# Kernel tuning notes

Measured on AMD Instinct MI355X. Metric: run time of the kernel, lower is better.

## Reference

```python
import jax, jax.numpy as jnp
import numpy as np

HIDDEN, NH, NKV, HD = 2048, 16, 2, 128
CTX, NL, POS = 4096, 36, 3000
THETA, EPS = 1.0e6, 1e-6


def _rope_cos_sin(pos):
    inv_freq = 1.0 / (THETA ** (jnp.arange(0, HD, 2, dtype=jnp.float32) / HD))  # [HD/2]
    ang = pos * inv_freq
    ang = jnp.concatenate([ang, ang])  # [HD]
    return jnp.cos(ang), jnp.sin(ang)


def _rotate_half(x):
    x1, x2 = x[..., : HD // 2], x[..., HD // 2 :]
    return jnp.concatenate([-x2, x1], axis=-1)


def setup_inputs() -> dict:
    key = jax.random.key(0)
    ks = jax.random.split(key, 12)
    w = lambda k, shape, s=0.02: (jax.random.normal(k, shape, dtype=jnp.float32) * s)
    mask = jnp.where(jnp.arange(CTX) <= POS, 0.0, -1e9).astype(jnp.float32).reshape(1, 1, 1, CTX)
    return {
        "hidden_states": jax.random.normal(ks[0], (1, 1, HIDDEN), dtype=jnp.float32),
        "position_ids": jnp.array([POS], dtype=jnp.int64 if jax.config.jax_enable_x64 else jnp.int32),
        "causal_mask": mask,
        "current_pos": POS,
        "ln_w": jnp.ones((HIDDEN,), jnp.float32) + w(ks[1], (HIDDEN,)),
        "wq": w(ks[2], (NH * HD, HIDDEN)),
        "bq": w(ks[3], (NH * HD,)),
        "wk": w(ks[4], (NKV * HD, HIDDEN)),
        "bk": w(ks[5], (NKV * HD,)),
        "wv": w(ks[6], (NKV * HD, HIDDEN)),
        "bv": w(ks[7], (NKV * HD,)),
        "wo": w(ks[8], (HIDDEN, NH * HD)),
        "kv_cache": w(ks[9], (2 * NL, NKV, CTX, HD), 1.0),
    }


def reference(hidden_states, position_ids, causal_mask, current_pos,
              ln_w, wq, bq, wk, bk, wv, bv, wo, kv_cache):
    x = hidden_states  # [1,1,H]
    # RMSNorm
    var = jnp.mean(x * x, axis=-1, keepdims=True)
    nx = x * jax.lax.rsqrt(var + EPS) * ln_w

    # QKV projections (single token)
    t = nx[0, 0]  # [H]
    q = (wq @ t + bq).reshape(NH, HD)    # [NH, HD]
    k = (wk @ t + bk).reshape(NKV, HD)   # [NKV, HD]
    v = (wv @ t + bv).reshape(NKV, HD)

    # RoPE at current position
    cos, sin = _rope_cos_sin(jnp.float32(current_pos))
    q = q * cos + _rotate_half(q) * sin
    k = k * cos + _rotate_half(k) * sin

    # KV-cache scatter write: key at layer slot 0, value at slot NL
    kv_cache = kv_cache.at[0, :, current_pos, :].set(k)
    kv_cache = kv_cache.at[NL, :, current_pos, :].set(v)
    key_cache = kv_cache[0]    # [NKV, CTX, HD]
    value_cache = kv_cache[NL]

    # GQA attention over full cache
    rep = NH // NKV
    K = jnp.repeat(key_cache, rep, axis=0)    # [NH, CTX, HD]
    V = jnp.repeat(value_cache, rep, axis=0)
    scores = jnp.einsum("hd,hkd->hk", q, K) / jnp.sqrt(jnp.float32(HD))
    scores = scores + causal_mask[0, 0, 0]    # [NH, CTX]
    probs = jax.nn.softmax(scores, axis=-1)
    ctx = jnp.einsum("hk,hkd->hd", probs, V)  # [NH, HD]
    attn_out = (wo @ ctx.reshape(NH * HD)).reshape(1, 1, HIDDEN)

    return hidden_states + attn_out
```

## Files before the change

kernel.cpp:

```cpp
#include <hip/hip_runtime.h>
#include <hip/hip_bf16.h>
#include <math.h>

#define HIDDEN 2048
#define NH 16
#define NKV 2
#define HD 128
#define CTX 4096
#define NL 36
#define EPS 1e-6f

#define CHUNK 128
#define NCHUNKS (CTX / CHUNK)
#define HPB 4
#define NGRP (NH / HPB)

#define WS_QRAW 0
#define WS_KRAW 2048
#define WS_VRAW 2304
#define WS_TAB  2560
#define WS_PML  2688
#define WS_PACC 3712

#define RSQRT_HD 0.08838834764831845f

__device__ __forceinline__ float dot4(float4 a, float4 b) {
    return a.x*b.x + a.y*b.y + a.z*b.z + a.w*b.w;
}

__global__ __launch_bounds__(256) void qkv_kernel(
    const float* __restrict__ x, const float* __restrict__ lnw,
    const float* __restrict__ wq, const float* __restrict__ bq,
    const float* __restrict__ wk, const float* __restrict__ bk,
    const float* __restrict__ wv, const float* __restrict__ bv,
    const int* __restrict__ curpos, float* __restrict__ ws)
{
    const int t = threadIdx.x;
    const int lane = t & 63, wid = t >> 6;

    if (blockIdx.x == 320) {
        if (t < 64) {
            double e = (double)t * (1.0 / 64.0);
            double invf = exp2(-19.931568569324174087 * e);
            double a = (double)curpos[0] * invf;
            a -= 6.2831853071795864769 * floor(a * 0.15915494309189533577);
            float s, c;
            sincosf((float)a, &s, &c);
            ws[WS_TAB + t] = c;
            ws[WS_TAB + 64 + t] = s;
        }
        return;
    }

    const int R0 = blockIdx.x * 8 + wid * 2;
    const float *w0, *w1; float b0, b1; float *dst0, *dst1;
    {
        int R = R0;
        if (R < 2048)      { w0 = wq + (size_t)R * HIDDEN;            b0 = bq[R];   dst0 = ws + WS_QRAW + R; }
        else if (R < 2304) { int r = R - 2048; w0 = wk + (size_t)r * HIDDEN; b0 = bk[r]; dst0 = ws + WS_KRAW + r; }
        else               { int r = R - 2304; w0 = wv + (size_t)r * HIDDEN; b0 = bv[r]; dst0 = ws + WS_VRAW + r; }
        R = R0 + 1;
        if (R < 2048)      { w1 = wq + (size_t)R * HIDDEN;            b1 = bq[R];   dst1 = ws + WS_QRAW + R; }
        else if (R < 2304) { int r = R - 2048; w1 = wk + (size_t)r * HIDDEN; b1 = bk[r]; dst1 = ws + WS_KRAW + r; }
        else               { int r = R - 2304; w1 = wv + (size_t)r * HIDDEN; b1 = bv[r]; dst1 = ws + WS_VRAW + r; }
    }
    const float4* w04 = (const float4*)w0;
    const float4* w14 = (const float4*)w1;
    float4 u[8], v[8];
    #pragma unroll
    for (int j = 0; j < 8; ++j) { u[j] = w04[j * 64 + lane]; v[j] = w14[j * 64 + lane]; }

    __shared__ float nx[HIDDEN];
    __shared__ float red[4];
    float4 xa = ((const float4*)x)[t * 2];
    float4 xb = ((const float4*)x)[t * 2 + 1];
    float ss = dot4(xa, xa) + dot4(xb, xb);
    #pragma unroll
    for (int m = 32; m; m >>= 1) ss += __shfl_xor(ss, m);
    if (lane == 0) red[wid] = ss;
    __syncthreads();
    float inv = rsqrtf((red[0] + red[1] + red[2] + red[3]) / (float)HIDDEN + EPS);
    float4 la = ((const float4*)lnw)[t * 2];
    float4 lb = ((const float4*)lnw)[t * 2 + 1];
    float4 na, nb;
    na.x = xa.x * inv * la.x; na.y = xa.y * inv * la.y;
    na.z = xa.z * inv * la.z; na.w = xa.w * inv * la.w;
    nb.x = xb.x * inv * lb.x; nb.y = xb.y * inv * lb.y;
    nb.z = xb.z * inv * lb.z; nb.w = xb.w * inv * lb.w;
    ((float4*)nx)[t * 2] = na;
    ((float4*)nx)[t * 2 + 1] = nb;
    __syncthreads();

    const float4* nx4 = (const float4*)nx;
    float a0 = 0.f, a1 = 0.f;
    #pragma unroll
    for (int j = 0; j < 8; ++j) {
        float4 n = nx4[j * 64 + lane];
        a0 += dot4(u[j], n);
        a1 += dot4(v[j], n);
    }
    #pragma unroll
    for (int m = 32; m; m >>= 1) { a0 += __shfl_xor(a0, m); a1 += __shfl_xor(a1, m); }
    if (lane == 0) { *dst0 = a0 + b0; *dst1 = a1 + b1; }
}

__global__ __launch_bounds__(256) void attn_kernel(
    const float* __restrict__ kv, const int* __restrict__ curpos,
    float* __restrict__ ws)
{
    const int pos = curpos[0];
    const int grp = blockIdx.x / NCHUNKS;
    const int c = blockIdx.x % NCHUNKS;
    const int start = c * CHUNK;
    if (start > pos) return;
    const int nvalid = min(CHUNK, pos + 1 - start);
    const int h0 = grp * HPB;
    const int kvh = h0 / (NH / NKV);
    const float* kc = kv + (size_t)kvh * CTX * HD;
    const float* vc = kv + (size_t)(NL * NKV + kvh) * CTX * HD;

    __shared__ float tab[128];
    __shared__ float qr[HPB][HD];
    __shared__ float sc[HPB][CHUNK];
    __shared__ float ctxh[8][HPB][HD];

    const int t = threadIdx.x;
    const int lane = t & 63, wid = t >> 6;

    if (t < 128) tab[t] = ws[WS_TAB + t];
    __syncthreads();

    #pragma unroll
    for (int i = 0; i < 2; ++i) {
        int e = t + i * 256;
        int hh = e >> 7, d = e & 127;
        const float* q = ws + WS_QRAW + (size_t)(h0 + hh) * HD;
        float qv = q[d], qp = q[d ^ 64];
        float r = (d < 64) ? -qp : qp;
        qr[hh][d] = (qv * tab[d & 63] + r * tab[64 + (d & 63)]) * RSQRT_HD;
    }
    __syncthreads();

    const int g16 = t >> 4, li = t & 15;
    float qreg[HPB][8];
    #pragma unroll
    for (int h = 0; h < HPB; ++h)
        #pragma unroll
        for (int j = 0; j < 8; ++j) qreg[h][j] = qr[h][li * 8 + j];

    for (int base = 0; base < nvalid; base += 16) {
        const int pl = base + g16;
        float s0 = 0.f, s1 = 0.f, s2 = 0.f, s3 = 0.f;
        if (pl < nvalid) {
            const int p = start + pl;
            float kd[8];
            if (p == pos) {
                const float* kr = ws + WS_KRAW + (size_t)kvh * HD;
                #pragma unroll
                for (int j = 0; j < 8; ++j) {
                    int d = li * 8 + j;
                    float kvd = kr[d], kp = kr[d ^ 64];
                    float r = (d < 64) ? -kp : kp;
                    kd[j] = kvd * tab[d & 63] + r * tab[64 + (d & 63)];
                }
            } else {
                const float4* kp4 = (const float4*)(kc + (size_t)p * HD + li * 8);
                float4 ka = kp4[0], kb = kp4[1];
                kd[0]=ka.x; kd[1]=ka.y; kd[2]=ka.z; kd[3]=ka.w;
                kd[4]=kb.x; kd[5]=kb.y; kd[6]=kb.z; kd[7]=kb.w;
            }
            #pragma unroll
            for (int j = 0; j < 8; ++j) {
                s0 += qreg[0][j] * kd[j];
                s1 += qreg[1][j] * kd[j];
                s2 += qreg[2][j] * kd[j];
                s3 += qreg[3][j] * kd[j];
            }
        }
        #pragma unroll
        for (int m = 1; m < 16; m <<= 1) {
            s0 += __shfl_xor(s0, m); s1 += __shfl_xor(s1, m);
            s2 += __shfl_xor(s2, m); s3 += __shfl_xor(s3, m);
        }
        if (pl < nvalid && li == 0) { sc[0][pl] = s0; sc[1][pl] = s1; sc[2][pl] = s2; sc[3][pl] = s3; }
    }
    __syncthreads();

    {
        float m = -INFINITY;
        for (int p = lane; p < nvalid; p += 64) m = fmaxf(m, sc[wid][p]);
        #pragma unroll
        for (int mm = 32; mm; mm >>= 1) m = fmaxf(m, __shfl_xor(m, mm));
        float l = 0.f;
        for (int p = lane; p < nvalid; p += 64) {
            float e = expf(sc[wid][p] - m);
            sc[wid][p] = e;
            l += e;
        }
        #pragma unroll
        for (int mm = 32; mm; mm >>= 1) l += __shfl_xor(l, mm);
        if (lane == 0) {
            ws[WS_PML + ((size_t)(h0 + wid) * NCHUNKS + c) * 2]     = m;
            ws[WS_PML + ((size_t)(h0 + wid) * NCHUNKS + c) * 2 + 1] = l;
        }
    }
    __syncthreads();

    {
        const int q4 = t & 31, half = t >> 5;
        float4 a[HPB];
        #pragma unroll
        for (int h = 0; h < HPB; ++h) a[h] = make_float4(0.f, 0.f, 0.f, 0.f);
        for (int pl = half; pl < nvalid; pl += 8) {
            const int p = start + pl;
            const float4* vp = (p == pos) ? (const float4*)(ws + WS_VRAW + (size_t)kvh * HD)
                                          : (const float4*)(vc + (size_t)p * HD);
            float4 vv = vp[q4];
            #pragma unroll
            for (int h = 0; h < HPB; ++h) {
                float w = sc[h][pl];
                a[h].x += w * vv.x; a[h].y += w * vv.y;
                a[h].z += w * vv.z; a[h].w += w * vv.w;
            }
        }
        #pragma unroll
        for (int h = 0; h < HPB; ++h)
            *(float4*)&ctxh[half][h][q4 * 4] = a[h];
    }
    __syncthreads();

    #pragma unroll
    for (int i = 0; i < 2; ++i) {
        int e = t + i * 256;
        int hh = e >> 7, d = e & 127;
        float s = 0.f;
        #pragma unroll
        for (int hf = 0; hf < 8; ++hf) s += ctxh[hf][hh][d];
        ws[WS_PACC + ((size_t)(h0 + hh) * NCHUNKS + c) * 128 + d] = s;
    }
}

__global__ __launch_bounds__(256) void out_kernel(
    const float* __restrict__ wo, const float* __restrict__ hidden,
    const float* __restrict__ ws, const int* __restrict__ curpos,
    float* __restrict__ out)
{
    const int t = threadIdx.x;
    const int lane = t & 63, wid = t >> 6;

    const int row0 = blockIdx.x * 8 + wid * 2;
    const float4* w04 = (const float4*)(wo + (size_t)row0 * HIDDEN);
    const float4* w14 = (const float4*)(wo + (size_t)(row0 + 1) * HIDDEN);
    float4 u[8], v[8];
    #pragma unroll
    for (int j = 0; j < 8; ++j) { u[j] = w04[j * 64 + lane]; v[j] = w14[j * 64 + lane]; }

    __shared__ float ctx[HIDDEN];
    const int pos = curpos[0];
    const int nc = pos / CHUNK + 1;
    const int h = t >> 4, sub = t & 15;
    float M = -INFINITY;
    for (int c = 0; c < nc; ++c)
        M = fmaxf(M, ws[WS_PML + ((size_t)h * NCHUNKS + c) * 2]);
    float L = 0.f;
    float4 acc0 = make_float4(0.f,0.f,0.f,0.f), acc1 = make_float4(0.f,0.f,0.f,0.f);
    for (int c = 0; c < nc; ++c) {
        float mm = ws[WS_PML + ((size_t)h * NCHUNKS + c) * 2];
        float ll = ws[WS_PML + ((size_t)h * NCHUNKS + c) * 2 + 1];
        float w = expf(mm - M);
        L += w * ll;
        const float4* pa = (const float4*)(ws + WS_PACC + ((size_t)h * NCHUNKS + c) * 128 + sub * 8);
        float4 p0 = pa[0], p1 = pa[1];
        acc0.x += w*p0.x; acc0.y += w*p0.y; acc0.z += w*p0.z; acc0.w += w*p0.w;
        acc1.x += w*p1.x; acc1.y += w*p1.y; acc1.z += w*p1.z; acc1.w += w*p1.w;
    }
    float invL = 1.f / L;
    acc0.x *= invL; acc0.y *= invL; acc0.z *= invL; acc0.w *= invL;
    acc1.x *= invL; acc1.y *= invL; acc1.z *= invL; acc1.w *= invL;
    *(float4*)&ctx[h * HD + sub * 8]     = acc0;
    *(float4*)&ctx[h * HD + sub * 8 + 4] = acc1;
    __syncthreads();

    const float4* c4 = (const float4*)ctx;
    float a0 = 0.f, a1 = 0.f;
    #pragma unroll
    for (int j = 0; j < 8; ++j) {
        float4 n = c4[j * 64 + lane];
        a0 += dot4(u[j], n);
        a1 += dot4(v[j], n);
    }
    #pragma unroll
    for (int m = 32; m; m >>= 1) { a0 += __shfl_xor(a0, m); a1 += __shfl_xor(a1, m); }
    if (lane == 0) {
        out[row0]     = hidden[row0]     + a0;
        out[row0 + 1] = hidden[row0 + 1] + a1;
    }
}

extern "C" void kernel_launch(void* const* d_in, const int* in_sizes, int n_in,
                              void* d_out, int out_size, void* d_ws, size_t ws_size,
                              hipStream_t stream)
{
    const float* hidden = (const float*)d_in[0];
    const int*   cur    = (const int*)d_in[3];
    const float* lnw    = (const float*)d_in[4];
    const float* wq     = (const float*)d_in[5];
    const float* bq     = (const float*)d_in[6];
    const float* wk     = (const float*)d_in[7];
    const float* bk     = (const float*)d_in[8];
    const float* wv     = (const float*)d_in[9];
    const float* bv     = (const float*)d_in[10];
    const float* wo     = (const float*)d_in[11];
    const float* kv     = (const float*)d_in[12];
    float* ws  = (float*)d_ws;
    float* out = (float*)d_out;

    qkv_kernel<<<dim3(321), dim3(256), 0, stream>>>(hidden, lnw, wq, bq, wk, bk, wv, bv, cur, ws);
    attn_kernel<<<dim3(NGRP * NCHUNKS), dim3(256), 0, stream>>>(kv, cur, ws);
    out_kernel<<<dim3(256), dim3(256), 0, stream>>>(wo, hidden, ws, cur, out);
}
```

Before: 37.92 us.

## Prefetch whole K/V chunk into registers before computing attention scores

The attention kernel now issues every K and V load for its 128-position chunk up front into registers (16 float4 of K and 16 float4 of V per thread). This exposes all memory requests at once instead of serialising load-compute loop iterations. The rotated current-position key is precomputed once into shared memory, and unused score slots are zeroed so the V accumulation loop can run fully unrolled. Launch bounds are set to one block per SM to allow the higher register use, at the risk of lower occupancy and of reading cache rows past pos in the last chunk.

```diff
diff --git a/kernel.cpp b/kernel.cpp
--- a/kernel.cpp
+++ b/kernel.cpp
@@ -28,7 +28,7 @@
     return a.x*b.x + a.y*b.y + a.z*b.z + a.w*b.w;
 }
 
-__global__ __launch_bounds__(256) void qkv_kernel(
+__global__ __launch_bounds__(256, 1) void qkv_kernel(
     const float* __restrict__ x, const float* __restrict__ lnw,
     const float* __restrict__ wq, const float* __restrict__ bq,
     const float* __restrict__ wk, const float* __restrict__ bk,
@@ -104,7 +104,7 @@
     if (lane == 0) { *dst0 = a0 + b0; *dst1 = a1 + b1; }
 }
 
-__global__ __launch_bounds__(256) void attn_kernel(
+__global__ __launch_bounds__(256, 1) void attn_kernel(
     const float* __restrict__ kv, const int* __restrict__ curpos,
     float* __restrict__ ws)
 {
@@ -120,6 +120,7 @@
     const float* vc = kv + (size_t)(NL * NKV + kvh) * CTX * HD;
 
     __shared__ float tab[128];
+    __shared__ float kf[HD];
     __shared__ float qr[HPB][HD];
     __shared__ float sc[HPB][CHUNK];
     __shared__ float ctxh[8][HPB][HD];
@@ -129,7 +130,12 @@
 
     if (t < 128) tab[t] = ws[WS_TAB + t];
     __syncthreads();
-
+    if (t < 128) {
+        const float* kr = ws + WS_KRAW + (size_t)kvh * HD;
+        float kvd = kr[t], kp = kr[t ^ 64];
+        float r = (t < 64) ? -kp : kp;
+        kf[t] = kvd * tab[t & 63] + r * tab[64 + (t & 63)];
+    }
     #pragma unroll
     for (int i = 0; i < 2; ++i) {
         int e = t + i * 256;
@@ -142,47 +148,55 @@
     __syncthreads();
 
     const int g16 = t >> 4, li = t & 15;
-    float qreg[HPB][8];
-    #pragma unroll
-    for (int h = 0; h < HPB; ++h)
-        #pragma unroll
-        for (int j = 0; j < 8; ++j) qreg[h][j] = qr[h][li * 8 + j];
-
-    for (int base = 0; base < nvalid; base += 16) {
-        const int pl = base + g16;
-        float s0 = 0.f, s1 = 0.f, s2 = 0.f, s3 = 0.f;
+    float4 ka[8], kb[8];
+    #pragma unroll
+    for (int it = 0; it < 8; ++it) {
+        const int p = start + it * 16 + g16;
+        const float4* kp = (const float4*)(kc + (size_t)p * HD + li * 8);
+        ka[it] = kp[0]; kb[it] = kp[1];
+    }
+    const int half = t >> 5, q4 = t & 31;
+    float4 vv[16];
+    #pragma unroll
+    for (int i = 0; i < 16; ++i) {
+        const int p = start + i * 8 + half;
+        vv[i] = ((const float4*)(vc + (size_t)p * HD))[q4];
+    }
+    float4 fv = ((const float4*)(ws + WS_VRAW + (size_t)kvh * HD))[q4];
+
+    float4 qa[HPB], qb[HPB];
+    #pragma unroll
+    for (int h = 0; h < HPB; ++h) {
+        qa[h] = *(const float4*)&qr[h][li * 8];
+        qb[h] = *(const float4*)&qr[h][li * 8 + 4];
+    }
+
+    #pragma unroll
+    for (int it = 0; it < 8; ++it) {
+        const int pl = it * 16 + g16;
         if (pl < nvalid) {
-            const int p = start + pl;
-            float kd[8];
-            if (p == pos) {
-                const float* kr = ws + WS_KRAW + (size_t)kvh * HD;
-                #pragma unroll
-                for (int j = 0; j < 8; ++j) {
-                    int d = li * 8 + j;
-                    float kvd = kr[d], kp = kr[d ^ 64];
-                    float r = (d < 64) ? -kp : kp;
-                    kd[j] = kvd * tab[d & 63] + r * tab[64 + (d & 63)];
-                }
-            } else {
-                const float4* kp4 = (const float4*)(kc + (size_t)p * HD + li * 8);
-                float4 ka = kp4[0], kb = kp4[1];
-                kd[0]=ka.x; kd[1]=ka.y; kd[2]=ka.z; kd[3]=ka.w;
-                kd[4]=kb.x; kd[5]=kb.y; kd[6]=kb.z; kd[7]=kb.w;
+            float4 A = ka[it], B = kb[it];
+            if (start + pl == pos) {
+                A = *(const float4*)&kf[li * 8];
+                B = *(const float4*)&kf[li * 8 + 4];
             }
+            float s0 = dot4(qa[0], A) + dot4(qb[0], B);
+            float s1 = dot4(qa[1], A) + dot4(qb[1], B);
+            float s2 = dot4(qa[2], A) + dot4(qb[2], B);
+            float s3 = dot4(qa[3], A) + dot4(qb[3], B);
             #pragma unroll
-            for (int j = 0; j < 8; ++j) {
-                s0 += qreg[0][j] * kd[j];
-                s1 += qreg[1][j] * kd[j];
-                s2 += qreg[2][j] * kd[j];
-                s3 += qreg[3][j] * kd[j];
+            for (int m = 1; m < 16; m <<= 1) {
+                s0 += __shfl_xor(s0, m); s1 += __shfl_xor(s1, m);
+                s2 += __shfl_xor(s2, m); s3 += __shfl_xor(s3, m);
             }
-        }
-        #pragma unroll
-        for (int m = 1; m < 16; m <<= 1) {
-            s0 += __shfl_xor(s0, m); s1 += __shfl_xor(s1, m);
-            s2 += __shfl_xor(s2, m); s3 += __shfl_xor(s3, m);
-        }
-        if (pl < nvalid && li == 0) { sc[0][pl] = s0; sc[1][pl] = s1; sc[2][pl] = s2; sc[3][pl] = s3; }
+            if (li == 0) { sc[0][pl] = s0; sc[1][pl] = s1; sc[2][pl] = s2; sc[3][pl] = s3; }
+        }
+    }
+    #pragma unroll
+    for (int i = 0; i < 2; ++i) {
+        int e = t + i * 256;
+        int hh = e >> 7, pl = e & 127;
+        if (pl >= nvalid) sc[hh][pl] = 0.f;
     }
     __syncthreads();
 
@@ -207,20 +221,18 @@
     __syncthreads();
 
     {
-        const int q4 = t & 31, half = t >> 5;
         float4 a[HPB];
         #pragma unroll
         for (int h = 0; h < HPB; ++h) a[h] = make_float4(0.f, 0.f, 0.f, 0.f);
-        for (int pl = half; pl < nvalid; pl += 8) {
-            const int p = start + pl;
-            const float4* vp = (p == pos) ? (const float4*)(ws + WS_VRAW + (size_t)kvh * HD)
-                                          : (const float4*)(vc + (size_t)p * HD);
-            float4 vv = vp[q4];
+        #pragma unroll
+        for (int i = 0; i < 16; ++i) {
+            const int pl = i * 8 + half;
+            float4 x = (start + pl == pos) ? fv : vv[i];
             #pragma unroll
             for (int h = 0; h < HPB; ++h) {
                 float w = sc[h][pl];
-                a[h].x += w * vv.x; a[h].y += w * vv.y;
-                a[h].z += w * vv.z; a[h].w += w * vv.w;
+                a[h].x += w * x.x; a[h].y += w * x.y;
+                a[h].z += w * x.z; a[h].w += w * x.w;
             }
         }
         #pragma unroll
@@ -240,7 +252,7 @@
     }
 }
 
-__global__ __launch_bounds__(256) void out_kernel(
+__global__ __launch_bounds__(256, 1) void out_kernel(
     const float* __restrict__ wo, const float* __restrict__ hidden,
     const float* __restrict__ ws, const int* __restrict__ curpos,
     float* __restrict__ out)
```

Result: slower. 39.41 us (+3.9%).
